# Performance work log

Hardware: AMD Instinct MI355X
Metric: run time of the kernel (lower is better)

Reference implementation:

```python
import jax, jax.numpy as jnp
import numpy as np

SEQ_LEN = 8192
EMBED_DIM = 768
OUTPUT_DIM = 64


def setup_inputs() -> dict:
    key = jax.random.key(0)
    k_in, k_q, k_k, k_v = jax.random.split(key, 4)
    inputs = jax.random.normal(k_in, (SEQ_LEN, EMBED_DIM), dtype=jnp.float32)
    W_Q = jax.random.normal(k_q, (EMBED_DIM, OUTPUT_DIM), dtype=jnp.float32)
    W_K = jax.random.normal(k_k, (EMBED_DIM, OUTPUT_DIM), dtype=jnp.float32)
    W_V = jax.random.normal(k_v, (EMBED_DIM, OUTPUT_DIM), dtype=jnp.float32)
    return {"inputs": inputs, "W_Q": W_Q, "W_K": W_K, "W_V": W_V}


def reference(inputs, W_Q, W_K, W_V):
    # inputs: [N, E]; weights: [E, D]
    queries = inputs @ W_Q              # [N, D]
    keys = inputs @ W_K                 # [N, D]
    values = inputs @ W_V               # [N, D]
    scale = values.shape[-1] ** 0.5     # sqrt(output_dim), as in the original
    scores = queries @ keys.T           # [N, N] -- full score matrix, as original
    weights = jax.nn.softmax(scores / scale, axis=-1)
    context = weights @ values          # [N, D]
    return context
```

## Files before the change

### kernel.cpp

```cpp
#include <hip/hip_runtime.h>
#include <hip/hip_fp16.h>

#define N_SEQ 8192
#define E_DIM 768
#define D_OUT 64
#define PADK 68
#define SCALE_LOG2 0.18033688011112042f

typedef __attribute__((ext_vector_type(8)))  short s16x8;
typedef __attribute__((ext_vector_type(4)))  float f32x4;
typedef __attribute__((ext_vector_type(16))) float f32x16;

static __device__ __forceinline__ unsigned short f2bf(float f) {
    union { float f; unsigned int u; } v; v.f = f;
    unsigned int r = v.u + 0x7FFFu + ((v.u >> 16) & 1u);
    return (unsigned short)(r >> 16);
}
static __device__ __forceinline__ float bf2f(unsigned short h) {
    union { float f; unsigned int u; } v; v.u = ((unsigned int)h) << 16; return v.f;
}
static __device__ __forceinline__ unsigned int packbf(float a, float b) {
    union { float f; unsigned int u; } x, y; x.f = a; y.f = b;
    return (y.u & 0xFFFF0000u) | (x.u >> 16);
}
static __device__ __forceinline__ s16x8 gfrag(const unsigned short* p) {
    union { uint4 u; s16x8 s; } r; r.u = *(const uint4*)p; return r.s;
}
static __device__ __forceinline__ s16x8 ldsfrag(const unsigned short* p) {
    union { uint2 u[2]; s16x8 s; } r;
    r.u[0] = *(const uint2*)(p);
    r.u[1] = *(const uint2*)(p + 4);
    return r.s;
}
static __device__ __forceinline__ void st32(unsigned short* d, uint4 a, uint4 b) {
    uint2* p = (uint2*)d;
    p[0] = make_uint2(a.x, a.y); p[1] = make_uint2(a.z, a.w);
    p[2] = make_uint2(b.x, b.y); p[3] = make_uint2(b.z, b.w);
}

__global__ __launch_bounds__(256) void prep_w(const float* __restrict__ WQ,
                                              const float* __restrict__ WK,
                                              const float* __restrict__ WV,
                                              unsigned short* __restrict__ Wthi,
                                              unsigned short* __restrict__ Wtlo) {
    int idx = blockIdx.x * 256 + threadIdx.x;
    if (idx >= 192 * E_DIM) return;
    int n = idx / E_DIM;
    int k = idx - n * E_DIM;
    float v;
    if (n < 64)       v = WQ[k * 64 + n];
    else if (n < 128) v = WK[k * 64 + (n - 64)];
    else              v = WV[k * 64 + (n - 128)];
    unsigned short hb = f2bf(v);
    Wthi[idx] = hb;
    Wtlo[idx] = f2bf(v - bf2f(hb));
}

__global__ __launch_bounds__(256) void prep_x(const float* __restrict__ X,
                                              unsigned short* __restrict__ Xhi,
                                              unsigned short* __restrict__ Xlo) {
    int idx = blockIdx.x * 256 + threadIdx.x;
    float4 v = ((const float4*)X)[idx];
    ushort4 hi, lo;
    hi.x = f2bf(v.x); lo.x = f2bf(v.x - bf2f(hi.x));
    hi.y = f2bf(v.y); lo.y = f2bf(v.y - bf2f(hi.y));
    hi.z = f2bf(v.z); lo.z = f2bf(v.z - bf2f(hi.z));
    hi.w = f2bf(v.w); lo.w = f2bf(v.w - bf2f(hi.w));
    ((ushort4*)Xhi)[idx] = hi;
    ((ushort4*)Xlo)[idx] = lo;
}

__global__ __launch_bounds__(256, 4) void proj_qkv(const unsigned short* __restrict__ Xhi,
                                                   const unsigned short* __restrict__ Xlo,
                                                   const unsigned short* __restrict__ Wthi,
                                                   const unsigned short* __restrict__ Wtlo,
                                                   unsigned short* __restrict__ Qhi,
                                                   unsigned short* __restrict__ Qlo,
                                                   unsigned short* __restrict__ Khi,
                                                   unsigned short* __restrict__ Klo,
                                                   unsigned short* __restrict__ Vt) {
    int tid  = threadIdx.x;
    int wv   = tid >> 6;
    int lane = tid & 63;
    int id   = blockIdx.x * 4 + wv;
    int mt   = id >> 2;
    int c    = id & 3;
    int m0 = mt * 16, n0 = c * 16;
    int lr = lane & 15, lk = lane >> 4;

    f32x4 aQ, aK, aV;
    #pragma unroll
    for (int i = 0; i < 4; ++i) { aQ[i] = 0.f; aK[i] = 0.f; aV[i] = 0.f; }

    const unsigned short* xh  = Xhi  + (size_t)(m0 + lr) * E_DIM + lk * 8;
    const unsigned short* xl  = Xlo  + (size_t)(m0 + lr) * E_DIM + lk * 8;
    const unsigned short* wqh = Wthi + (size_t)(n0 + lr) * E_DIM + lk * 8;
    const unsigned short* wql = Wtlo + (size_t)(n0 + lr) * E_DIM + lk * 8;
    const unsigned short* wkh = Wthi + (size_t)(64 + n0 + lr) * E_DIM + lk * 8;
    const unsigned short* wkl = Wtlo + (size_t)(64 + n0 + lr) * E_DIM + lk * 8;
    const unsigned short* wvh = Wthi + (size_t)(128 + n0 + lr) * E_DIM + lk * 8;

    #pragma unroll 2
    for (int ks = 0; ks < E_DIM / 32; ++ks) {
        int kb = ks * 32;
        s16x8 ah = gfrag(xh + kb);
        s16x8 al = gfrag(xl + kb);
        s16x8 bqh = gfrag(wqh + kb);
        s16x8 bql = gfrag(wql + kb);
        s16x8 bkh = gfrag(wkh + kb);
        s16x8 bkl = gfrag(wkl + kb);
        s16x8 bvh = gfrag(wvh + kb);
        aQ = __builtin_amdgcn_mfma_f32_16x16x32_bf16(ah, bqh, aQ, 0, 0, 0);
        aK = __builtin_amdgcn_mfma_f32_16x16x32_bf16(ah, bkh, aK, 0, 0, 0);
        aV = __builtin_amdgcn_mfma_f32_16x16x32_bf16(ah, bvh, aV, 0, 0, 0);
        aQ = __builtin_amdgcn_mfma_f32_16x16x32_bf16(ah, bql, aQ, 0, 0, 0);
        aK = __builtin_amdgcn_mfma_f32_16x16x32_bf16(ah, bkl, aK, 0, 0, 0);
        aQ = __builtin_amdgcn_mfma_f32_16x16x32_bf16(al, bqh, aQ, 0, 0, 0);
        aK = __builtin_amdgcn_mfma_f32_16x16x32_bf16(al, bkh, aK, 0, 0, 0);
    }

    #pragma unroll
    for (int r = 0; r < 4; ++r) {
        int grow = m0 + lk * 4 + r, gcol = n0 + lr;
        float q = aQ[r] * SCALE_LOG2;
        unsigned short hb = f2bf(q);
        Qhi[(size_t)grow * 64 + gcol] = hb;
        Qlo[(size_t)grow * 64 + gcol] = f2bf(q - bf2f(hb));
        float v = aK[r];
        hb = f2bf(v);
        Khi[(size_t)grow * 64 + gcol] = hb;
        Klo[(size_t)grow * 64 + gcol] = f2bf(v - bf2f(hb));
    }
    ushort4 pk;
    pk.x = f2bf(aV[0]); pk.y = f2bf(aV[1]);
    pk.z = f2bf(aV[2]); pk.w = f2bf(aV[3]);
    *(ushort4*)(Vt + (size_t)(n0 + lr) * N_SEQ + m0 + lk * 4) = pk;
}

__global__ __launch_bounds__(256, 3) void attn(const unsigned short* __restrict__ Qhi,
                                               const unsigned short* __restrict__ Qlo,
                                               const unsigned short* __restrict__ Khi,
                                               const unsigned short* __restrict__ Klo,
                                               const unsigned short* __restrict__ Vt,
                                               float* __restrict__ Opart,
                                               float* __restrict__ mpart,
                                               float* __restrict__ lpart,
                                               int chunk) {
    __shared__ unsigned short sK[128 * PADK];
    __shared__ unsigned short sV [64 * PADK];

    int tid = threadIdx.x, wv = tid >> 6, lane = tid & 63;
    int lrow = lane & 31, lh = lane >> 5;
    int c = blockIdx.x, qb = blockIdx.y;
    int q0 = qb * 128 + wv * 32;

    s16x8 qh[4], ql[4];
    #pragma unroll
    for (int ks = 0; ks < 4; ++ks) {
        int kb = ks * 16 + lh * 8;
        qh[ks] = gfrag(Qhi + (size_t)(q0 + lrow) * 64 + kb);
        ql[ks] = gfrag(Qlo + (size_t)(q0 + lrow) * 64 + kb);
    }

    f32x16 O0, O1;
    #pragma unroll
    for (int i = 0; i < 16; ++i) { O0[i] = 0.f; O1[i] = 0.f; }
    float mrow = -1e30f, lrun = 0.f;

    int steps = chunk >> 6;
    int srow = tid >> 2, sseg = tid & 3;

    uint4 rA0, rA1, rB0, rB1, rC0, rC1;
    {
        int j1 = c * chunk;
        const uint4* ps = (const uint4*)(Khi + ((size_t)(j1 + srow) * 64 + sseg * 16));
        rA0 = ps[0]; rA1 = ps[1];
        ps = (const uint4*)(Klo + ((size_t)(j1 + srow) * 64 + sseg * 16));
        rB0 = ps[0]; rB1 = ps[1];
        ps = (const uint4*)(Vt + ((size_t)srow * N_SEQ + j1 + sseg * 16));
        rC0 = ps[0]; rC1 = ps[1];
    }

    for (int it = 0; it < steps; ++it) {
        __syncthreads();
        st32(sK + srow * PADK + sseg * 16, rA0, rA1);
        st32(sK + (64 + srow) * PADK + sseg * 16, rB0, rB1);
        st32(sV + srow * PADK + sseg * 16, rC0, rC1);
        __syncthreads();

        if (it + 1 < steps) {
            int j1 = c * chunk + (it + 1) * 64;
            const uint4* ps = (const uint4*)(Khi + ((size_t)(j1 + srow) * 64 + sseg * 16));
            rA0 = ps[0]; rA1 = ps[1];
            ps = (const uint4*)(Klo + ((size_t)(j1 + srow) * 64 + sseg * 16));
            rB0 = ps[0]; rB1 = ps[1];
            ps = (const uint4*)(Vt + ((size_t)srow * N_SEQ + j1 + sseg * 16));
            rC0 = ps[0]; rC1 = ps[1];
        }

        f32x16 s0, s1;
        #pragma unroll
        for (int i = 0; i < 16; ++i) { s0[i] = 0.f; s1[i] = 0.f; }
        #pragma unroll
        for (int ks = 0; ks < 4; ++ks) {
            int kb = ks * 16 + lh * 8;
            s16x8 b0h = ldsfrag(sK + (size_t)lrow * PADK + kb);
            s16x8 b0l = ldsfrag(sK + (size_t)(64 + lrow) * PADK + kb);
            s0 = __builtin_amdgcn_mfma_f32_32x32x16_bf16(b0h, qh[ks], s0, 0, 0, 0);
            s0 = __builtin_amdgcn_mfma_f32_32x32x16_bf16(b0l, qh[ks], s0, 0, 0, 0);
            s0 = __builtin_amdgcn_mfma_f32_32x32x16_bf16(b0h, ql[ks], s0, 0, 0, 0);
            s16x8 b1h = ldsfrag(sK + (size_t)(32 + lrow) * PADK + kb);
            s16x8 b1l = ldsfrag(sK + (size_t)(96 + lrow) * PADK + kb);
            s1 = __builtin_amdgcn_mfma_f32_32x32x16_bf16(b1h, qh[ks], s1, 0, 0, 0);
            s1 = __builtin_amdgcn_mfma_f32_32x32x16_bf16(b1l, qh[ks], s1, 0, 0, 0);
            s1 = __builtin_amdgcn_mfma_f32_32x32x16_bf16(b1h, ql[ks], s1, 0, 0, 0);
        }

        float rm = s0[0];
        #pragma unroll
        for (int i = 1; i < 16; ++i) rm = fmaxf(rm, s0[i]);
        #pragma unroll
        for (int i = 0; i < 16; ++i) rm = fmaxf(rm, s1[i]);
        rm = fmaxf(rm, __shfl_xor(rm, 32, 64));
        float mn  = fmaxf(mrow, rm);
        float alf = exp2f(mrow - mn);
        mrow = mn;

        float psum = 0.f;
        #pragma unroll
        for (int i = 0; i < 16; ++i) { s0[i] = exp2f(s0[i] - mn); psum += s0[i]; }
        #pragma unroll
        for (int i = 0; i < 16; ++i) { s1[i] = exp2f(s1[i] - mn); psum += s1[i]; }
        lrun = lrun * alf + psum;

        unsigned int I[16], J[16];
        #pragma unroll
        for (int q4 = 0; q4 < 4; ++q4) {
            I[2 * q4]     = packbf(s0[4 * q4],     s0[4 * q4 + 1]);
            I[2 * q4 + 1] = packbf(s0[4 * q4 + 2], s0[4 * q4 + 3]);
            I[8 + 2 * q4]     = packbf(s1[4 * q4],     s1[4 * q4 + 1]);
            I[8 + 2 * q4 + 1] = packbf(s1[4 * q4 + 2], s1[4 * q4 + 3]);
        }
        #pragma unroll
        for (int i = 0; i < 16; ++i) J[i] = (unsigned int)__shfl_xor((int)I[i], 32, 64);
        s16x8 a[4];
        #pragma unroll
        for (int ks = 0; ks < 4; ++ks) {
            int b = (ks >> 1) * 8 + (ks & 1) * 4;
            union { unsigned int u[4]; s16x8 s; } fa;
            fa.u[0] = lh ? J[b + 2] : I[b];
            fa.u[1] = lh ? J[b + 3] : I[b + 1];
            fa.u[2] = lh ? I[b + 2] : J[b];
            fa.u[3] = lh ? I[b + 3] : J[b + 1];
            a[ks] = fa.s;
        }

        #pragma unroll
        for (int r = 0; r < 16; ++r) {
            int qr = (r & 3) + 8 * (r >> 2) + 4 * lh;
            float af = __shfl(alf, qr, 64);
            O0[r] *= af; O1[r] *= af;
        }

        #pragma unroll
        for (int ks = 0; ks < 4; ++ks) {
            int kb = ks * 16 + lh * 8;
            s16x8 b0 = ldsfrag(sV + (size_t)lrow * PADK + kb);
            s16x8 b1 = ldsfrag(sV + (size_t)(32 + lrow) * PADK + kb);
            O0 = __builtin_amdgcn_mfma_f32_32x32x16_bf16(a[ks], b0, O0, 0, 0, 0);
            O1 = __builtin_amdgcn_mfma_f32_32x32x16_bf16(a[ks], b1, O1, 0, 0, 0);
        }
    }

    #pragma unroll
    for (int r = 0; r < 16; ++r) {
        int row = (r & 3) + 8 * (r >> 2) + 4 * lh;
        int grow = q0 + row;
        size_t ob = ((size_t)c * N_SEQ + grow) * 64;
        Opart[ob + lrow]      = O0[r];
        Opart[ob + 32 + lrow] = O1[r];
    }
    float lfull = lrun + __shfl_xor(lrun, 32, 64);
    if (lane < 32) {
        int grow = q0 + lrow;
        mpart[c * N_SEQ + grow] = mrow;
        lpart[c * N_SEQ + grow] = lfull;
    }
}

__global__ __launch_bounds__(256) void combine(const float* __restrict__ Opart,
                                               const float* __restrict__ mpart,
                                               const float* __restrict__ lpart,
                                               float* __restrict__ out,
                                               int nsplit) {
    int idx = blockIdx.x * 256 + threadIdx.x;
    int row = idx >> 4, d4 = idx & 15;
    float M = -1e30f;
    for (int c = 0; c < nsplit; ++c) M = fmaxf(M, mpart[c * N_SEQ + row]);
    float4 num = make_float4(0.f, 0.f, 0.f, 0.f);
    float den = 0.f;
    for (int c = 0; c < nsplit; ++c) {
        float w = exp2f(mpart[c * N_SEQ + row] - M);
        den += w * lpart[c * N_SEQ + row];
        float4 o = ((const float4*)Opart)[((size_t)c * N_SEQ + row) * 16 + d4];
        num.x += w * o.x; num.y += w * o.y; num.z += w * o.z; num.w += w * o.w;
    }
    float inv = 1.0f / den;
    num.x *= inv; num.y *= inv; num.z *= inv; num.w *= inv;
    ((float4*)out)[idx] = num;
}

extern "C" void kernel_launch(void* const* d_in, const int* in_sizes, int n_in,
                              void* d_out, int out_size, void* d_ws, size_t ws_size,
                              hipStream_t stream) {
    const float* X  = (const float*)d_in[0];
    const float* WQ = (const float*)d_in[1];
    const float* WK = (const float*)d_in[2];
    const float* WV = (const float*)d_in[3];
    float* out = (float*)d_out;

    const size_t szQK = (size_t)N_SEQ * 64 * 2;
    const size_t szW  = (size_t)192 * E_DIM * 2;
    const size_t szX  = (size_t)N_SEQ * E_DIM * 2;
    char* p = (char*)d_ws;
    unsigned short* Qhi = (unsigned short*)p; p += szQK;
    unsigned short* Qlo = (unsigned short*)p; p += szQK;
    unsigned short* Khi = (unsigned short*)p; p += szQK;
    unsigned short* Klo = (unsigned short*)p; p += szQK;
    unsigned short* Vt  = (unsigned short*)p; p += szQK;
    unsigned short* Wthi = (unsigned short*)p; p += szW;
    unsigned short* Wtlo = (unsigned short*)p; p += szW;
    unsigned short* Xhi = (unsigned short*)p; p += szX;
    unsigned short* Xlo = (unsigned short*)p; p += szX;
    size_t base = (size_t)(p - (char*)d_ws);
    size_t per  = (size_t)N_SEQ * 64 * 4 + 2 * (size_t)N_SEQ * 4;
    int nsplit = 16;
    while (nsplit > 1 && base + (size_t)nsplit * per > ws_size) nsplit >>= 1;
    float* mpart = (float*)p; p += (size_t)nsplit * N_SEQ * 4;
    float* lpart = (float*)p; p += (size_t)nsplit * N_SEQ * 4;
    float* Opart = (float*)p;

    int chunk = N_SEQ / nsplit;

    prep_w<<<(192 * E_DIM + 255) / 256, 256, 0, stream>>>(WQ, WK, WV, Wthi, Wtlo);
    prep_x<<<(N_SEQ * E_DIM / 4) / 256, 256, 0, stream>>>(X, Xhi, Xlo);
    proj_qkv<<<512, 256, 0, stream>>>(Xhi, Xlo, Wthi, Wtlo, Qhi, Qlo, Khi, Klo, Vt);
    attn<<<dim3(nsplit, N_SEQ / 128), 256, 0, stream>>>(Qhi, Qlo, Khi, Klo, Vt,
                                                        Opart, mpart, lpart, chunk);
    combine<<<(N_SEQ * 16 + 255) / 256, 256, 0, stream>>>(Opart, mpart, lpart, out, nsplit);
}
```

Measured before the change: 177.3 us.

## Shrink attention blocks to two waves, add lazy rescaling and faster softmax reductions

The attention kernel now uses 128-thread blocks covering 64 query rows, and each thread stages twice as much K/V data into shared memory per step. The online softmax skips rescaling the output accumulators unless some row max grows by more than 8 (in log2 units), and the max and sum reductions are split into several independent chains. bf16 packing becomes a single byte-permute instruction. Smaller blocks mean K/V tiles are reloaded by twice as many blocks, and the deferred rescale lets exponentials grow up to 2^8 before renormalising.

```diff
diff --git a/kernel.cpp b/kernel.cpp
--- a/kernel.cpp
+++ b/kernel.cpp
@@ -19,10 +19,6 @@
 static __device__ __forceinline__ float bf2f(unsigned short h) {
     union { float f; unsigned int u; } v; v.u = ((unsigned int)h) << 16; return v.f;
 }
-static __device__ __forceinline__ unsigned int packbf(float a, float b) {
-    union { float f; unsigned int u; } x, y; x.f = a; y.f = b;
-    return (y.u & 0xFFFF0000u) | (x.u >> 16);
-}
 static __device__ __forceinline__ s16x8 gfrag(const unsigned short* p) {
     union { uint4 u; s16x8 s; } r; r.u = *(const uint4*)p; return r.s;
 }
@@ -32,10 +28,15 @@
     r.u[1] = *(const uint2*)(p + 4);
     return r.s;
 }
-static __device__ __forceinline__ void st32(unsigned short* d, uint4 a, uint4 b) {
+static __device__ __forceinline__ unsigned int packbf(float a, float b) {
+    return __builtin_amdgcn_perm(__float_as_uint(b), __float_as_uint(a), 0x07060302u);
+}
+static __device__ __forceinline__ void st64(unsigned short* d, const uint4* r) {
     uint2* p = (uint2*)d;
-    p[0] = make_uint2(a.x, a.y); p[1] = make_uint2(a.z, a.w);
-    p[2] = make_uint2(b.x, b.y); p[3] = make_uint2(b.z, b.w);
+    p[0] = make_uint2(r[0].x, r[0].y); p[1] = make_uint2(r[0].z, r[0].w);
+    p[2] = make_uint2(r[1].x, r[1].y); p[3] = make_uint2(r[1].z, r[1].w);
+    p[4] = make_uint2(r[2].x, r[2].y); p[5] = make_uint2(r[2].z, r[2].w);
+    p[6] = make_uint2(r[3].x, r[3].y); p[7] = make_uint2(r[3].z, r[3].w);
 }
 
 __global__ __launch_bounds__(256) void prep_w(const float* __restrict__ WQ,
@@ -137,7 +138,7 @@
     *(ushort4*)(Vt + (size_t)(n0 + lr) * N_SEQ + m0 + lk * 4) = pk;
 }
 
-__global__ __launch_bounds__(256, 3) void attn(const unsigned short* __restrict__ Qhi,
+__global__ __launch_bounds__(128, 3) void attn(const unsigned short* __restrict__ Qhi,
                                                const unsigned short* __restrict__ Qlo,
                                                const unsigned short* __restrict__ Khi,
                                                const unsigned short* __restrict__ Klo,
@@ -152,7 +153,7 @@
     int tid = threadIdx.x, wv = tid >> 6, lane = tid & 63;
     int lrow = lane & 31, lh = lane >> 5;
     int c = blockIdx.x, qb = blockIdx.y;
-    int q0 = qb * 128 + wv * 32;
+    int q0 = qb * 64 + wv * 32;
 
     s16x8 qh[4], ql[4];
     #pragma unroll
@@ -168,34 +169,34 @@
     float mrow = -1e30f, lrun = 0.f;
 
     int steps = chunk >> 6;
-    int srow = tid >> 2, sseg = tid & 3;
-
-    uint4 rA0, rA1, rB0, rB1, rC0, rC1;
+    int srow = tid >> 1, sseg = tid & 1;
+
+    uint4 rA[4], rB[4], rC[4];
     {
         int j1 = c * chunk;
-        const uint4* ps = (const uint4*)(Khi + ((size_t)(j1 + srow) * 64 + sseg * 16));
-        rA0 = ps[0]; rA1 = ps[1];
-        ps = (const uint4*)(Klo + ((size_t)(j1 + srow) * 64 + sseg * 16));
-        rB0 = ps[0]; rB1 = ps[1];
-        ps = (const uint4*)(Vt + ((size_t)srow * N_SEQ + j1 + sseg * 16));
-        rC0 = ps[0]; rC1 = ps[1];
+        const uint4* ps = (const uint4*)(Khi + ((size_t)(j1 + srow) * 64 + sseg * 32));
+        rA[0] = ps[0]; rA[1] = ps[1]; rA[2] = ps[2]; rA[3] = ps[3];
+        ps = (const uint4*)(Klo + ((size_t)(j1 + srow) * 64 + sseg * 32));
+        rB[0] = ps[0]; rB[1] = ps[1]; rB[2] = ps[2]; rB[3] = ps[3];
+        ps = (const uint4*)(Vt + ((size_t)srow * N_SEQ + j1 + sseg * 32));
+        rC[0] = ps[0]; rC[1] = ps[1]; rC[2] = ps[2]; rC[3] = ps[3];
     }
 
     for (int it = 0; it < steps; ++it) {
         __syncthreads();
-        st32(sK + srow * PADK + sseg * 16, rA0, rA1);
-        st32(sK + (64 + srow) * PADK + sseg * 16, rB0, rB1);
-        st32(sV + srow * PADK + sseg * 16, rC0, rC1);
+        st64(sK + srow * PADK + sseg * 32, rA);
+        st64(sK + (64 + srow) * PADK + sseg * 32, rB);
+        st64(sV + srow * PADK + sseg * 32, rC);
         __syncthreads();
 
         if (it + 1 < steps) {
             int j1 = c * chunk + (it + 1) * 64;
-            const uint4* ps = (const uint4*)(Khi + ((size_t)(j1 + srow) * 64 + sseg * 16));
-            rA0 = ps[0]; rA1 = ps[1];
-            ps = (const uint4*)(Klo + ((size_t)(j1 + srow) * 64 + sseg * 16));
-            rB0 = ps[0]; rB1 = ps[1];
-            ps = (const uint4*)(Vt + ((size_t)srow * N_SEQ + j1 + sseg * 16));
-            rC0 = ps[0]; rC1 = ps[1];
+            const uint4* ps = (const uint4*)(Khi + ((size_t)(j1 + srow) * 64 + sseg * 32));
+            rA[0] = ps[0]; rA[1] = ps[1]; rA[2] = ps[2]; rA[3] = ps[3];
+            ps = (const uint4*)(Klo + ((size_t)(j1 + srow) * 64 + sseg * 32));
+            rB[0] = ps[0]; rB[1] = ps[1]; rB[2] = ps[2]; rB[3] = ps[3];
+            ps = (const uint4*)(Vt + ((size_t)srow * N_SEQ + j1 + sseg * 32));
+            rC[0] = ps[0]; rC[1] = ps[1]; rC[2] = ps[2]; rC[3] = ps[3];
         }
 
         f32x16 s0, s1;
@@ -216,22 +217,47 @@
             s1 = __builtin_amdgcn_mfma_f32_32x32x16_bf16(b1h, ql[ks], s1, 0, 0, 0);
         }
 
-        float rm = s0[0];
-        #pragma unroll
-        for (int i = 1; i < 16; ++i) rm = fmaxf(rm, s0[i]);
-        #pragma unroll
-        for (int i = 0; i < 16; ++i) rm = fmaxf(rm, s1[i]);
+        float r0 = fmaxf(s0[0], s1[0]), r1 = fmaxf(s0[1], s1[1]);
+        float r2 = fmaxf(s0[2], s1[2]), r3 = fmaxf(s0[3], s1[3]);
+        #pragma unroll
+        for (int i = 4; i < 16; i += 4) {
+            r0 = fmaxf(r0, fmaxf(s0[i],     s1[i]));
+            r1 = fmaxf(r1, fmaxf(s0[i + 1], s1[i + 1]));
+            r2 = fmaxf(r2, fmaxf(s0[i + 2], s1[i + 2]));
+            r3 = fmaxf(r3, fmaxf(s0[i + 3], s1[i + 3]));
+        }
+        float rm = fmaxf(fmaxf(r0, r1), fmaxf(r2, r3));
         rm = fmaxf(rm, __shfl_xor(rm, 32, 64));
-        float mn  = fmaxf(mrow, rm);
-        float alf = exp2f(mrow - mn);
-        mrow = mn;
-
-        float psum = 0.f;
-        #pragma unroll
-        for (int i = 0; i < 16; ++i) { s0[i] = exp2f(s0[i] - mn); psum += s0[i]; }
-        #pragma unroll
-        for (int i = 0; i < 16; ++i) { s1[i] = exp2f(s1[i] - mn); psum += s1[i]; }
-        lrun = lrun * alf + psum;
+
+        if (__any(rm > mrow + 8.0f)) {
+            float mn  = fmaxf(mrow, rm);
+            float alf = exp2f(mrow - mn);
+            mrow = mn;
+            lrun *= alf;
+            #pragma unroll
+            for (int r = 0; r < 16; ++r) {
+                int qr = (r & 3) + 8 * (r >> 2) + 4 * lh;
+                float af = __shfl(alf, qr, 64);
+                O0[r] *= af; O1[r] *= af;
+            }
+        }
+
+        float p0 = 0.f, p1 = 0.f, p2 = 0.f, p3 = 0.f;
+        #pragma unroll
+        for (int i = 0; i < 16; i += 4) {
+            s0[i]     = exp2f(s0[i] - mrow);     p0 += s0[i];
+            s0[i + 1] = exp2f(s0[i + 1] - mrow); p1 += s0[i + 1];
+            s0[i + 2] = exp2f(s0[i + 2] - mrow); p2 += s0[i + 2];
+            s0[i + 3] = exp2f(s0[i + 3] - mrow); p3 += s0[i + 3];
+        }
+        #pragma unroll
+        for (int i = 0; i < 16; i += 4) {
+            s1[i]     = exp2f(s1[i] - mrow);     p0 += s1[i];
+            s1[i + 1] = exp2f(s1[i + 1] - mrow); p1 += s1[i + 1];
+            s1[i + 2] = exp2f(s1[i + 2] - mrow); p2 += s1[i + 2];
+            s1[i + 3] = exp2f(s1[i + 3] - mrow); p3 += s1[i + 3];
+        }
+        lrun += (p0 + p1) + (p2 + p3);
 
         unsigned int I[16], J[16];
         #pragma unroll
@@ -253,13 +279,6 @@
             fa.u[2] = lh ? I[b + 2] : J[b];
             fa.u[3] = lh ? I[b + 3] : J[b + 1];
             a[ks] = fa.s;
-        }
-
-        #pragma unroll
-        for (int r = 0; r < 16; ++r) {
-            int qr = (r & 3) + 8 * (r >> 2) + 4 * lh;
-            float af = __shfl(alf, qr, 64);
-            O0[r] *= af; O1[r] *= af;
         }
 
         #pragma unroll
@@ -345,7 +364,7 @@
     prep_w<<<(192 * E_DIM + 255) / 256, 256, 0, stream>>>(WQ, WK, WV, Wthi, Wtlo);
     prep_x<<<(N_SEQ * E_DIM / 4) / 256, 256, 0, stream>>>(X, Xhi, Xlo);
     proj_qkv<<<512, 256, 0, stream>>>(Xhi, Xlo, Wthi, Wtlo, Qhi, Qlo, Khi, Klo, Vt);
-    attn<<<dim3(nsplit, N_SEQ / 128), 256, 0, stream>>>(Qhi, Qlo, Khi, Klo, Vt,
-                                                        Opart, mpart, lpart, chunk);
+    attn<<<dim3(nsplit, N_SEQ / 64), 128, 0, stream>>>(Qhi, Qlo, Khi, Klo, Vt,
+                                                       Opart, mpart, lpart, chunk);
     combine<<<(N_SEQ * 16 + 255) / 256, 256, 0, stream>>>(Opart, mpart, lpart, out, nsplit);
 }
```

Result: slower. 201.4 us (+13.6%).

## Merge prep kernels, shrink proj blocks, lazy softmax rescale, split MFMA accumulators

Applied to the files above, without the earlier changes.

Merges the two prep kernels into one launch and relaunches proj_qkv as 2048 single-wave blocks. In the attention loop it splits the score accumulators so the hi and lo MFMA chains run independently, and uses tree-style max and sum reductions. The output rescale is skipped unless a row max grows by more than 8 in log2 units, which saves shuffles and multiplies. It also uses a perm intrinsic for bf16 packing and raises the attention occupancy hint to 4. The extra accumulators raise register pressure, which may conflict with the higher occupancy target.

```diff
diff --git a/kernel.cpp b/kernel.cpp
--- a/kernel.cpp
+++ b/kernel.cpp
@@ -19,10 +19,6 @@
 static __device__ __forceinline__ float bf2f(unsigned short h) {
     union { float f; unsigned int u; } v; v.u = ((unsigned int)h) << 16; return v.f;
 }
-static __device__ __forceinline__ unsigned int packbf(float a, float b) {
-    union { float f; unsigned int u; } x, y; x.f = a; y.f = b;
-    return (y.u & 0xFFFF0000u) | (x.u >> 16);
-}
 static __device__ __forceinline__ s16x8 gfrag(const unsigned short* p) {
     union { uint4 u; s16x8 s; } r; r.u = *(const uint4*)p; return r.s;
 }
@@ -32,57 +28,60 @@
     r.u[1] = *(const uint2*)(p + 4);
     return r.s;
 }
+static __device__ __forceinline__ unsigned int packbf(float a, float b) {
+    return __builtin_amdgcn_perm(__float_as_uint(b), __float_as_uint(a), 0x07060302u);
+}
 static __device__ __forceinline__ void st32(unsigned short* d, uint4 a, uint4 b) {
     uint2* p = (uint2*)d;
     p[0] = make_uint2(a.x, a.y); p[1] = make_uint2(a.z, a.w);
     p[2] = make_uint2(b.x, b.y); p[3] = make_uint2(b.z, b.w);
 }
 
-__global__ __launch_bounds__(256) void prep_w(const float* __restrict__ WQ,
-                                              const float* __restrict__ WK,
-                                              const float* __restrict__ WV,
-                                              unsigned short* __restrict__ Wthi,
-                                              unsigned short* __restrict__ Wtlo) {
-    int idx = blockIdx.x * 256 + threadIdx.x;
-    if (idx >= 192 * E_DIM) return;
-    int n = idx / E_DIM;
-    int k = idx - n * E_DIM;
-    float v;
-    if (n < 64)       v = WQ[k * 64 + n];
-    else if (n < 128) v = WK[k * 64 + (n - 64)];
-    else              v = WV[k * 64 + (n - 128)];
-    unsigned short hb = f2bf(v);
-    Wthi[idx] = hb;
-    Wtlo[idx] = f2bf(v - bf2f(hb));
-}
-
-__global__ __launch_bounds__(256) void prep_x(const float* __restrict__ X,
-                                              unsigned short* __restrict__ Xhi,
-                                              unsigned short* __restrict__ Xlo) {
-    int idx = blockIdx.x * 256 + threadIdx.x;
-    float4 v = ((const float4*)X)[idx];
-    ushort4 hi, lo;
-    hi.x = f2bf(v.x); lo.x = f2bf(v.x - bf2f(hi.x));
-    hi.y = f2bf(v.y); lo.y = f2bf(v.y - bf2f(hi.y));
-    hi.z = f2bf(v.z); lo.z = f2bf(v.z - bf2f(hi.z));
-    hi.w = f2bf(v.w); lo.w = f2bf(v.w - bf2f(hi.w));
-    ((ushort4*)Xhi)[idx] = hi;
-    ((ushort4*)Xlo)[idx] = lo;
-}
-
-__global__ __launch_bounds__(256, 4) void proj_qkv(const unsigned short* __restrict__ Xhi,
-                                                   const unsigned short* __restrict__ Xlo,
-                                                   const unsigned short* __restrict__ Wthi,
-                                                   const unsigned short* __restrict__ Wtlo,
-                                                   unsigned short* __restrict__ Qhi,
-                                                   unsigned short* __restrict__ Qlo,
-                                                   unsigned short* __restrict__ Khi,
-                                                   unsigned short* __restrict__ Klo,
-                                                   unsigned short* __restrict__ Vt) {
-    int tid  = threadIdx.x;
-    int wv   = tid >> 6;
-    int lane = tid & 63;
-    int id   = blockIdx.x * 4 + wv;
+__global__ __launch_bounds__(256) void prep(const float* __restrict__ X,
+                                            const float* __restrict__ WQ,
+                                            const float* __restrict__ WK,
+                                            const float* __restrict__ WV,
+                                            unsigned short* __restrict__ Xhi,
+                                            unsigned short* __restrict__ Xlo,
+                                            unsigned short* __restrict__ Wthi,
+                                            unsigned short* __restrict__ Wtlo) {
+    int bx = blockIdx.x;
+    if (bx < 6144) {
+        int idx = bx * 256 + threadIdx.x;
+        float4 v = ((const float4*)X)[idx];
+        ushort4 hi, lo;
+        hi.x = f2bf(v.x); lo.x = f2bf(v.x - bf2f(hi.x));
+        hi.y = f2bf(v.y); lo.y = f2bf(v.y - bf2f(hi.y));
+        hi.z = f2bf(v.z); lo.z = f2bf(v.z - bf2f(hi.z));
+        hi.w = f2bf(v.w); lo.w = f2bf(v.w - bf2f(hi.w));
+        ((ushort4*)Xhi)[idx] = hi;
+        ((ushort4*)Xlo)[idx] = lo;
+    } else {
+        int idx = (bx - 6144) * 256 + threadIdx.x;
+        if (idx >= 192 * E_DIM) return;
+        int n = idx / E_DIM;
+        int k = idx - n * E_DIM;
+        float v;
+        if (n < 64)       v = WQ[k * 64 + n];
+        else if (n < 128) v = WK[k * 64 + (n - 64)];
+        else              v = WV[k * 64 + (n - 128)];
+        unsigned short hb = f2bf(v);
+        Wthi[idx] = hb;
+        Wtlo[idx] = f2bf(v - bf2f(hb));
+    }
+}
+
+__global__ __launch_bounds__(64, 4) void proj_qkv(const unsigned short* __restrict__ Xhi,
+                                                  const unsigned short* __restrict__ Xlo,
+                                                  const unsigned short* __restrict__ Wthi,
+                                                  const unsigned short* __restrict__ Wtlo,
+                                                  unsigned short* __restrict__ Qhi,
+                                                  unsigned short* __restrict__ Qlo,
+                                                  unsigned short* __restrict__ Khi,
+                                                  unsigned short* __restrict__ Klo,
+                                                  unsigned short* __restrict__ Vt) {
+    int lane = threadIdx.x;
+    int id   = blockIdx.x;
     int mt   = id >> 2;
     int c    = id & 3;
     int m0 = mt * 16, n0 = c * 16;
@@ -137,7 +136,7 @@
     *(ushort4*)(Vt + (size_t)(n0 + lr) * N_SEQ + m0 + lk * 4) = pk;
 }
 
-__global__ __launch_bounds__(256, 3) void attn(const unsigned short* __restrict__ Qhi,
+__global__ __launch_bounds__(256, 4) void attn(const unsigned short* __restrict__ Qhi,
                                                const unsigned short* __restrict__ Qlo,
                                                const unsigned short* __restrict__ Khi,
                                                const unsigned short* __restrict__ Klo,
@@ -198,40 +197,67 @@
             rC0 = ps[0]; rC1 = ps[1];
         }
 
-        f32x16 s0, s1;
-        #pragma unroll
-        for (int i = 0; i < 16; ++i) { s0[i] = 0.f; s1[i] = 0.f; }
+        f32x16 sa0, sb0, sa1, sb1;
+        #pragma unroll
+        for (int i = 0; i < 16; ++i) { sa0[i] = 0.f; sb0[i] = 0.f; sa1[i] = 0.f; sb1[i] = 0.f; }
         #pragma unroll
         for (int ks = 0; ks < 4; ++ks) {
             int kb = ks * 16 + lh * 8;
             s16x8 b0h = ldsfrag(sK + (size_t)lrow * PADK + kb);
             s16x8 b0l = ldsfrag(sK + (size_t)(64 + lrow) * PADK + kb);
-            s0 = __builtin_amdgcn_mfma_f32_32x32x16_bf16(b0h, qh[ks], s0, 0, 0, 0);
-            s0 = __builtin_amdgcn_mfma_f32_32x32x16_bf16(b0l, qh[ks], s0, 0, 0, 0);
-            s0 = __builtin_amdgcn_mfma_f32_32x32x16_bf16(b0h, ql[ks], s0, 0, 0, 0);
+            sa0 = __builtin_amdgcn_mfma_f32_32x32x16_bf16(b0h, qh[ks], sa0, 0, 0, 0);
+            sb0 = __builtin_amdgcn_mfma_f32_32x32x16_bf16(b0l, qh[ks], sb0, 0, 0, 0);
+            sb0 = __builtin_amdgcn_mfma_f32_32x32x16_bf16(b0h, ql[ks], sb0, 0, 0, 0);
             s16x8 b1h = ldsfrag(sK + (size_t)(32 + lrow) * PADK + kb);
             s16x8 b1l = ldsfrag(sK + (size_t)(96 + lrow) * PADK + kb);
-            s1 = __builtin_amdgcn_mfma_f32_32x32x16_bf16(b1h, qh[ks], s1, 0, 0, 0);
-            s1 = __builtin_amdgcn_mfma_f32_32x32x16_bf16(b1l, qh[ks], s1, 0, 0, 0);
-            s1 = __builtin_amdgcn_mfma_f32_32x32x16_bf16(b1h, ql[ks], s1, 0, 0, 0);
-        }
-
-        float rm = s0[0];
-        #pragma unroll
-        for (int i = 1; i < 16; ++i) rm = fmaxf(rm, s0[i]);
-        #pragma unroll
-        for (int i = 0; i < 16; ++i) rm = fmaxf(rm, s1[i]);
+            sa1 = __builtin_amdgcn_mfma_f32_32x32x16_bf16(b1h, qh[ks], sa1, 0, 0, 0);
+            sb1 = __builtin_amdgcn_mfma_f32_32x32x16_bf16(b1l, qh[ks], sb1, 0, 0, 0);
+            sb1 = __builtin_amdgcn_mfma_f32_32x32x16_bf16(b1h, ql[ks], sb1, 0, 0, 0);
+        }
+        f32x16 s0 = sa0 + sb0;
+        f32x16 s1 = sa1 + sb1;
+
+        float r0 = fmaxf(s0[0], s1[0]), r1 = fmaxf(s0[1], s1[1]);
+        float r2 = fmaxf(s0[2], s1[2]), r3 = fmaxf(s0[3], s1[3]);
+        #pragma unroll
+        for (int i = 4; i < 16; i += 4) {
+            r0 = fmaxf(r0, fmaxf(s0[i],     s1[i]));
+            r1 = fmaxf(r1, fmaxf(s0[i + 1], s1[i + 1]));
+            r2 = fmaxf(r2, fmaxf(s0[i + 2], s1[i + 2]));
+            r3 = fmaxf(r3, fmaxf(s0[i + 3], s1[i + 3]));
+        }
+        float rm = fmaxf(fmaxf(r0, r1), fmaxf(r2, r3));
         rm = fmaxf(rm, __shfl_xor(rm, 32, 64));
-        float mn  = fmaxf(mrow, rm);
-        float alf = exp2f(mrow - mn);
-        mrow = mn;
-
-        float psum = 0.f;
-        #pragma unroll
-        for (int i = 0; i < 16; ++i) { s0[i] = exp2f(s0[i] - mn); psum += s0[i]; }
-        #pragma unroll
-        for (int i = 0; i < 16; ++i) { s1[i] = exp2f(s1[i] - mn); psum += s1[i]; }
-        lrun = lrun * alf + psum;
+
+        if (__any(rm > mrow + 8.0f)) {
+            float mn  = fmaxf(mrow, rm);
+            float alf = exp2f(mrow - mn);
+            mrow = mn;
+            lrun *= alf;
+            #pragma unroll
+            for (int r = 0; r < 16; ++r) {
+                int qr = (r & 3) + 8 * (r >> 2) + 4 * lh;
+                float af = __shfl(alf, qr, 64);
+                O0[r] *= af; O1[r] *= af;
+            }
+        }
+
+        float p0 = 0.f, p1 = 0.f, p2 = 0.f, p3 = 0.f;
+        #pragma unroll
+        for (int i = 0; i < 16; i += 4) {
+            s0[i]     = exp2f(s0[i] - mrow);     p0 += s0[i];
+            s0[i + 1] = exp2f(s0[i + 1] - mrow); p1 += s0[i + 1];
+            s0[i + 2] = exp2f(s0[i + 2] - mrow); p2 += s0[i + 2];
+            s0[i + 3] = exp2f(s0[i + 3] - mrow); p3 += s0[i + 3];
+        }
+        #pragma unroll
+        for (int i = 0; i < 16; i += 4) {
+            s1[i]     = exp2f(s1[i] - mrow);     p0 += s1[i];
+            s1[i + 1] = exp2f(s1[i + 1] - mrow); p1 += s1[i + 1];
+            s1[i + 2] = exp2f(s1[i + 2] - mrow); p2 += s1[i + 2];
+            s1[i + 3] = exp2f(s1[i + 3] - mrow); p3 += s1[i + 3];
+        }
+        lrun += (p0 + p1) + (p2 + p3);
 
         unsigned int I[16], J[16];
         #pragma unroll
@@ -253,13 +279,6 @@
             fa.u[2] = lh ? I[b + 2] : J[b];
             fa.u[3] = lh ? I[b + 3] : J[b + 1];
             a[ks] = fa.s;
-        }
-
-        #pragma unroll
-        for (int r = 0; r < 16; ++r) {
-            int qr = (r & 3) + 8 * (r >> 2) + 4 * lh;
-            float af = __shfl(alf, qr, 64);
-            O0[r] *= af; O1[r] *= af;
         }
 
         #pragma unroll
@@ -342,9 +361,9 @@
 
     int chunk = N_SEQ / nsplit;
 
-    prep_w<<<(192 * E_DIM + 255) / 256, 256, 0, stream>>>(WQ, WK, WV, Wthi, Wtlo);
-    prep_x<<<(N_SEQ * E_DIM / 4) / 256, 256, 0, stream>>>(X, Xhi, Xlo);
-    proj_qkv<<<512, 256, 0, stream>>>(Xhi, Xlo, Wthi, Wtlo, Qhi, Qlo, Khi, Klo, Vt);
+    prep<<<6144 + (192 * E_DIM + 255) / 256, 256, 0, stream>>>(X, WQ, WK, WV,
+                                                               Xhi, Xlo, Wthi, Wtlo);
+    proj_qkv<<<2048, 64, 0, stream>>>(Xhi, Xlo, Wthi, Wtlo, Qhi, Qlo, Khi, Klo, Vt);
     attn<<<dim3(nsplit, N_SEQ / 128), 256, 0, stream>>>(Qhi, Qlo, Khi, Klo, Vt,
                                                         Opart, mpart, lpart, chunk);
     combine<<<(N_SEQ * 16 + 255) / 256, 256, 0, stream>>>(Opart, mpart, lpart, out, nsplit);
```

Measured after the change: 276.8 us. 56.1% more time.
